# Kernel optimization log

Hardware: AMD Instinct MI355X
Metric: run time of the kernel (lower is better)

The kernel has to match this reference:

```python
import jax, jax.numpy as jnp
import numpy as np

B, N, D = 8, 256, 42   # batch, natoms, nFeatures
H1, H2 = 64, 32        # dmirror_FC hidden sizes


def setup_inputs() -> dict:
    key = jax.random.key(0)
    ks = jax.random.split(key, 8)
    s1, s2, s3 = (1.0 / np.sqrt(D)), (1.0 / np.sqrt(H1)), (1.0 / np.sqrt(H2))
    return {
        "image": jax.random.normal(ks[0], (B, N, D), dtype=jnp.float32),
        "dfeat": jax.random.normal(ks[1], (B, N, N, D, 3), dtype=jnp.float32),
        "W1": jax.random.normal(ks[2], (D, H1), dtype=jnp.float32) * s1,
        "b1": jax.random.normal(ks[3], (H1,), dtype=jnp.float32) * s1,
        "W2": jax.random.normal(ks[4], (H1, H2), dtype=jnp.float32) * s2,
        "b2": jax.random.normal(ks[5], (H2,), dtype=jnp.float32) * s2,
        "W3": jax.random.normal(ks[6], (H2, 1), dtype=jnp.float32) * s3,
        "b3": jax.random.normal(ks[7], (1,), dtype=jnp.float32) * s3,
    }


def reference(image, dfeat, W1, b1, W2, b2, W3, b3):
    # Per-atom mirrored MLP (dmirror_FC, softplus activation, d(softplus)=sigmoid),
    # fully vectorized over (batch, atom) instead of nested Python loops.
    z1 = image @ W1 + b1                 # [B,N,H1]
    a1 = jax.nn.softplus(z1)
    z2 = a1 @ W2 + b2                    # [B,N,H2]
    a2 = jax.nn.softplus(z2)
    Ei = (a2 @ W3 + b3)[..., 0]          # [B,N]
    Etot = jnp.sum(Ei, axis=1)           # [B]

    # Analytic mirrored backward: dEi/dFeat via chain rule
    g2 = jax.nn.sigmoid(z2) * W3[:, 0]   # [B,N,H2]
    g1 = jax.nn.sigmoid(z1) * (g2 @ W2.T)  # [B,N,H1]
    dEi_dFeat = g1 @ W1.T                # [B,N,D]

    # Force[b,i,:] = dEtot_dFeat[b] @ dfeat[b,i].reshape(N*D,3)
    Force = jnp.einsum('bjf,bijfc->bic', dEi_dFeat, dfeat)  # [B,N,3]
    return Etot, Force
```

## Files before the change

### kernel.cpp

```cpp
#include <hip/hip_runtime.h>

#define BATCH 8
#define NATOM 256
#define DF    42
#define H1    64
#define H2    32

__device__ __forceinline__ float softplus_f(float z) {
  return fmaxf(z, 0.f) + log1pf(expf(-fabsf(z)));
}

__global__ __launch_bounds__(256) void k1_mlp(
    const float* __restrict__ image,
    const float* __restrict__ W1, const float* __restrict__ b1,
    const float* __restrict__ W2, const float* __restrict__ b2,
    const float* __restrict__ W3, const float* __restrict__ b3,
    float* __restrict__ dG, float* __restrict__ Ei_ws) {
  __shared__ float sW1 [DF*H1];
  __shared__ float sW1T[H1*DF];
  __shared__ float sW2 [H1*H2];
  __shared__ float sW2T[H2*H1];
  __shared__ float sW3[H2], sb1[H1], sb2[H2];

  const int tid = threadIdx.x;
  for (int idx = tid; idx < DF*H1; idx += 256) {
    float w = W1[idx];
    sW1[idx] = w;
    sW1T[(idx & (H1-1))*DF + (idx >> 6)] = w;
  }
  for (int idx = tid; idx < H1*H2; idx += 256) {
    float w = W2[idx];
    sW2[idx] = w;
    sW2T[(idx & (H2-1))*H1 + (idx >> 5)] = w;
  }
  if (tid < H2)                    { sW3[tid] = W3[tid]; sb2[tid] = b2[tid]; }
  else if (tid >= 64 && tid < 128) { sb1[tid-64] = b1[tid-64]; }
  __syncthreads();

  const int lane = tid & 63;
  const int atom = blockIdx.x * 4 + (tid >> 6);

  float xv = (lane < DF) ? image[atom*DF + lane] : 0.f;

  float z1 = sb1[lane];
  #pragma unroll
  for (int d = 0; d < DF; ++d)
    z1 = fmaf(__shfl(xv, d), sW1[d*H1 + lane], z1);
  float a1 = softplus_f(z1);

  const int h2l = lane & (H2-1);
  float z2 = sb2[h2l];
  #pragma unroll
  for (int h = 0; h < H1; ++h)
    z2 = fmaf(__shfl(a1, h), sW2[h*H2 + h2l], z2);
  float a2 = softplus_f(z2);

  float w3  = sW3[h2l];
  float eip = a2 * w3;
  #pragma unroll
  for (int off = 16; off; off >>= 1) eip += __shfl_xor(eip, off);
  float g2 = (1.f - expf(-a2)) * w3;

  float t1 = 0.f;
  #pragma unroll
  for (int h2 = 0; h2 < H2; ++h2)
    t1 = fmaf(__shfl(g2, h2), sW2T[h2*H1 + lane], t1);
  float g1 = (1.f - expf(-a1)) * t1;

  const int dl = (lane < DF) ? lane : 0;
  float s = 0.f;
  #pragma unroll
  for (int h = 0; h < H1; ++h)
    s = fmaf(__shfl(g1, h), sW1T[h*DF + dl], s);

  if (lane < DF) dG[atom*DF + lane] = s;
  if (lane == 0) Ei_ws[atom] = eip + b3[0];
}

__global__ __launch_bounds__(256) void k2_force(
    const float* __restrict__ dfeat,
    const float* __restrict__ dG,
    const float* __restrict__ Ei_ws,
    float* __restrict__ out) {
  __shared__ float4 dg4[NATOM*DF/4];
  __shared__ float red[4][3];
  __shared__ float ered[4];

  const int tid = threadIdx.x;
  const int bid = blockIdx.x;
  const int b = bid >> 8;
  const int i = bid & 255;

  const float4* __restrict__ dgg = (const float4*)(dG + b*(NATOM*DF));
  for (int idx = tid; idx < NATOM*DF/4; idx += 256)
    dg4[idx] = dgg[idx];

  if (i == 0) {
    float e = Ei_ws[b*NATOM + tid];
    #pragma unroll
    for (int off = 32; off; off >>= 1) e += __shfl_down(e, off);
    if ((tid & 63) == 0) ered[tid >> 6] = e;
  }
  __syncthreads();
  if (i == 0 && tid == 0) out[b] = ered[0] + ered[1] + ered[2] + ered[3];

  const float4* __restrict__ p4 =
      (const float4*)(dfeat + (size_t)bid * (NATOM*DF*3));

  float ax = 0.f, ay = 0.f, az = 0.f;
  for (int u = tid; u < NATOM*DF*3/12; u += 256) {
    float4 v0 = p4[3*u + 0];
    float4 v1 = p4[3*u + 1];
    float4 v2 = p4[3*u + 2];
    float4 g  = dg4[u];
    ax += g.x*v0.x + g.y*v0.w + g.z*v1.z + g.w*v2.y;
    ay += g.x*v0.y + g.y*v1.x + g.z*v1.w + g.w*v2.z;
    az += g.x*v0.z + g.y*v1.y + g.z*v2.x + g.w*v2.w;
  }

  #pragma unroll
  for (int off = 32; off; off >>= 1) {
    ax += __shfl_down(ax, off);
    ay += __shfl_down(ay, off);
    az += __shfl_down(az, off);
  }
  const int wv = tid >> 6;
  if ((tid & 63) == 0) { red[wv][0] = ax; red[wv][1] = ay; red[wv][2] = az; }
  __syncthreads();
  if (tid == 0) {
    out[BATCH + (size_t)bid*3 + 0] = red[0][0]+red[1][0]+red[2][0]+red[3][0];
    out[BATCH + (size_t)bid*3 + 1] = red[0][1]+red[1][1]+red[2][1]+red[3][1];
    out[BATCH + (size_t)bid*3 + 2] = red[0][2]+red[1][2]+red[2][2]+red[3][2];
  }
}

extern "C" void kernel_launch(void* const* d_in, const int* in_sizes, int n_in,
                              void* d_out, int out_size, void* d_ws, size_t ws_size,
                              hipStream_t stream) {
  const float* image = (const float*)d_in[0];
  const float* dfeat = (const float*)d_in[1];
  const float* W1    = (const float*)d_in[2];
  const float* b1    = (const float*)d_in[3];
  const float* W2    = (const float*)d_in[4];
  const float* b2    = (const float*)d_in[5];
  const float* W3    = (const float*)d_in[6];
  const float* b3    = (const float*)d_in[7];
  float* out = (float*)d_out;

  float* dG = (float*)d_ws;
  float* Ei = dG + BATCH*NATOM*DF;

  k1_mlp<<<BATCH*NATOM/4, 256, 0, stream>>>(image, W1, b1, W2, b2, W3, b3, dG, Ei);
  k2_force<<<BATCH*NATOM, 256, 0, stream>>>(dfeat, dG, Ei, out);
}
```

Baseline: 62.72 us.

## Drop LDS staging of dG in force kernel, use nontemporal dfeat loads

Removes the per-block copy of the batch's dG vector into shared memory (43 KB) and the barrier that followed it; each thread now reads its dG slice directly from global/L2. The dfeat stream is read with nontemporal loads so it does not evict dG from cache, and the loop is fixed-count with a tail and unrolled by two. Dropping the large LDS allocation and adding launch bounds of 8 aims to raise occupancy for this bandwidth-bound streaming kernel. In exchange, every block re-reads dG from L2 instead of LDS, and the Etot write moves after the final barrier.

```diff
diff --git a/kernel.cpp b/kernel.cpp
--- a/kernel.cpp
+++ b/kernel.cpp
@@ -5,6 +5,8 @@
 #define DF    42
 #define H1    64
 #define H2    32
+
+typedef float f32x4 __attribute__((ext_vector_type(4)));
 
 __device__ __forceinline__ float softplus_f(float z) {
   return fmaxf(z, 0.f) + log1pf(expf(-fabsf(z)));
@@ -77,12 +79,11 @@
   if (lane == 0) Ei_ws[atom] = eip + b3[0];
 }
 
-__global__ __launch_bounds__(256) void k2_force(
+__global__ __launch_bounds__(256, 8) void k2_force(
     const float* __restrict__ dfeat,
     const float* __restrict__ dG,
     const float* __restrict__ Ei_ws,
     float* __restrict__ out) {
-  __shared__ float4 dg4[NATOM*DF/4];
   __shared__ float red[4][3];
   __shared__ float ered[4];
 
@@ -91,28 +92,35 @@
   const int b = bid >> 8;
   const int i = bid & 255;
 
-  const float4* __restrict__ dgg = (const float4*)(dG + b*(NATOM*DF));
-  for (int idx = tid; idx < NATOM*DF/4; idx += 256)
-    dg4[idx] = dgg[idx];
-
   if (i == 0) {
     float e = Ei_ws[b*NATOM + tid];
     #pragma unroll
     for (int off = 32; off; off >>= 1) e += __shfl_down(e, off);
     if ((tid & 63) == 0) ered[tid >> 6] = e;
   }
-  __syncthreads();
-  if (i == 0 && tid == 0) out[b] = ered[0] + ered[1] + ered[2] + ered[3];
 
-  const float4* __restrict__ p4 =
-      (const float4*)(dfeat + (size_t)bid * (NATOM*DF*3));
+  const f32x4* __restrict__ dgg = (const f32x4*)(dG + b*(NATOM*DF));
+  const f32x4* __restrict__ p4 =
+      (const f32x4*)(dfeat + (size_t)bid * (NATOM*DF*3));
 
   float ax = 0.f, ay = 0.f, az = 0.f;
-  for (int u = tid; u < NATOM*DF*3/12; u += 256) {
-    float4 v0 = p4[3*u + 0];
-    float4 v1 = p4[3*u + 1];
-    float4 v2 = p4[3*u + 2];
-    float4 g  = dg4[u];
+  #pragma unroll 2
+  for (int it = 0; it < 10; ++it) {
+    const int u = tid + it * 256;
+    f32x4 v0 = __builtin_nontemporal_load(p4 + 3*u + 0);
+    f32x4 v1 = __builtin_nontemporal_load(p4 + 3*u + 1);
+    f32x4 v2 = __builtin_nontemporal_load(p4 + 3*u + 2);
+    f32x4 g  = dgg[u];
+    ax += g.x*v0.x + g.y*v0.w + g.z*v1.z + g.w*v2.y;
+    ay += g.x*v0.y + g.y*v1.x + g.z*v1.w + g.w*v2.z;
+    az += g.x*v0.z + g.y*v1.y + g.z*v2.x + g.w*v2.w;
+  }
+  if (tid < 128) {
+    const int u = tid + 2560;
+    f32x4 v0 = __builtin_nontemporal_load(p4 + 3*u + 0);
+    f32x4 v1 = __builtin_nontemporal_load(p4 + 3*u + 1);
+    f32x4 v2 = __builtin_nontemporal_load(p4 + 3*u + 2);
+    f32x4 g  = dgg[u];
     ax += g.x*v0.x + g.y*v0.w + g.z*v1.z + g.w*v2.y;
     ay += g.x*v0.y + g.y*v1.x + g.z*v1.w + g.w*v2.z;
     az += g.x*v0.z + g.y*v1.y + g.z*v2.x + g.w*v2.w;
@@ -131,6 +139,7 @@
     out[BATCH + (size_t)bid*3 + 0] = red[0][0]+red[1][0]+red[2][0]+red[3][0];
     out[BATCH + (size_t)bid*3 + 1] = red[0][1]+red[1][1]+red[2][1]+red[3][1];
     out[BATCH + (size_t)bid*3 + 2] = red[0][2]+red[1][2]+red[2][2]+red[3][2];
+    if (i == 0) out[b] = ered[0] + ered[1] + ered[2] + ered[3];
   }
 }
 
```

New measurement: 78.66 us. +25.4%, slower.

## Process four force rows per 512-thread block to amortize dG shared staging

Applied to the files above, without the earlier changes.

The force kernel now uses 512-thread blocks, and each block computes four atoms' force rows instead of one. The per-batch dG vector is staged into LDS once per four rows, which cuts the repeated LDS staging and dG reads. Inner loops are fully unrolled with fixed trip counts, and a per-row wave reduction writes into a larger shared buffer. The grid shrinks to a quarter of the blocks, which may reduce latency hiding on a memory-bound streaming load of dfeat.

```diff
diff --git a/kernel.cpp b/kernel.cpp
--- a/kernel.cpp
+++ b/kernel.cpp
@@ -5,6 +5,8 @@
 #define DF    42
 #define H1    64
 #define H2    32
+
+typedef float f32x4 __attribute__((ext_vector_type(4)));
 
 __device__ __forceinline__ float softplus_f(float z) {
   return fmaxf(z, 0.f) + log1pf(expf(-fabsf(z)));
@@ -77,61 +79,80 @@
   if (lane == 0) Ei_ws[atom] = eip + b3[0];
 }
 
-__global__ __launch_bounds__(256) void k2_force(
+__global__ __launch_bounds__(512, 4) void k2_force(
     const float* __restrict__ dfeat,
     const float* __restrict__ dG,
     const float* __restrict__ Ei_ws,
     float* __restrict__ out) {
-  __shared__ float4 dg4[NATOM*DF/4];
-  __shared__ float red[4][3];
+  __shared__ f32x4 dgL[NATOM*DF/4];
+  __shared__ float red[4][8][3];
   __shared__ float ered[4];
 
   const int tid = threadIdx.x;
-  const int bid = blockIdx.x;
-  const int b = bid >> 8;
-  const int i = bid & 255;
+  const int blk = blockIdx.x;
+  const int b = blk >> 6;
 
-  const float4* __restrict__ dgg = (const float4*)(dG + b*(NATOM*DF));
-  for (int idx = tid; idx < NATOM*DF/4; idx += 256)
-    dg4[idx] = dgg[idx];
+  const f32x4* __restrict__ dgg = (const f32x4*)(dG + b*(NATOM*DF));
+  #pragma unroll
+  for (int m = 0; m < 5; ++m) dgL[tid + m*512] = dgg[tid + m*512];
+  if (tid < 128) dgL[tid + 2560] = dgg[tid + 2560];
 
-  if (i == 0) {
+  if ((blk & 63) == 0 && tid < 256) {
     float e = Ei_ws[b*NATOM + tid];
     #pragma unroll
     for (int off = 32; off; off >>= 1) e += __shfl_down(e, off);
     if ((tid & 63) == 0) ered[tid >> 6] = e;
   }
   __syncthreads();
-  if (i == 0 && tid == 0) out[b] = ered[0] + ered[1] + ered[2] + ered[3];
 
-  const float4* __restrict__ p4 =
-      (const float4*)(dfeat + (size_t)bid * (NATOM*DF*3));
+  const int wv = tid >> 6;
+  for (int r = 0; r < 4; ++r) {
+    const int R = blk*4 + r;
+    const f32x4* __restrict__ p4 = (const f32x4*)(dfeat + (size_t)R * (NATOM*DF*3));
 
-  float ax = 0.f, ay = 0.f, az = 0.f;
-  for (int u = tid; u < NATOM*DF*3/12; u += 256) {
-    float4 v0 = p4[3*u + 0];
-    float4 v1 = p4[3*u + 1];
-    float4 v2 = p4[3*u + 2];
-    float4 g  = dg4[u];
-    ax += g.x*v0.x + g.y*v0.w + g.z*v1.z + g.w*v2.y;
-    ay += g.x*v0.y + g.y*v1.x + g.z*v1.w + g.w*v2.z;
-    az += g.x*v0.z + g.y*v1.y + g.z*v2.x + g.w*v2.w;
+    float ax = 0.f, ay = 0.f, az = 0.f;
+    #pragma unroll
+    for (int m = 0; m < 5; ++m) {
+      const int g = tid + m*512;
+      f32x4 v0 = p4[3*g + 0];
+      f32x4 v1 = p4[3*g + 1];
+      f32x4 v2 = p4[3*g + 2];
+      f32x4 gg = dgL[g];
+      ax += gg.x*v0.x + gg.y*v0.w + gg.z*v1.z + gg.w*v2.y;
+      ay += gg.x*v0.y + gg.y*v1.x + gg.z*v1.w + gg.w*v2.z;
+      az += gg.x*v0.z + gg.y*v1.y + gg.z*v2.x + gg.w*v2.w;
+    }
+    if (tid < 128) {
+      const int g = tid + 2560;
+      f32x4 v0 = p4[3*g + 0];
+      f32x4 v1 = p4[3*g + 1];
+      f32x4 v2 = p4[3*g + 2];
+      f32x4 gg = dgL[g];
+      ax += gg.x*v0.x + gg.y*v0.w + gg.z*v1.z + gg.w*v2.y;
+      ay += gg.x*v0.y + gg.y*v1.x + gg.z*v1.w + gg.w*v2.z;
+      az += gg.x*v0.z + gg.y*v1.y + gg.z*v2.x + gg.w*v2.w;
+    }
+
+    #pragma unroll
+    for (int off = 32; off; off >>= 1) {
+      ax += __shfl_down(ax, off);
+      ay += __shfl_down(ay, off);
+      az += __shfl_down(az, off);
+    }
+    if ((tid & 63) == 0) { red[r][wv][0] = ax; red[r][wv][1] = ay; red[r][wv][2] = az; }
   }
 
-  #pragma unroll
-  for (int off = 32; off; off >>= 1) {
-    ax += __shfl_down(ax, off);
-    ay += __shfl_down(ay, off);
-    az += __shfl_down(az, off);
+  __syncthreads();
+  if (tid < 12) {
+    const int r = tid >> 2 == 0 ? tid / 3 : tid / 3;
+    const int c = tid - (tid/3)*3;
+    float s = 0.f;
+    #pragma unroll
+    for (int w = 0; w < 8; ++w) s += red[tid/3][w][c];
+    out[BATCH + (size_t)(blk*4 + tid/3)*3 + c] = s;
   }
-  const int wv = tid >> 6;
-  if ((tid & 63) == 0) { red[wv][0] = ax; red[wv][1] = ay; red[wv][2] = az; }
-  __syncthreads();
-  if (tid == 0) {
-    out[BATCH + (size_t)bid*3 + 0] = red[0][0]+red[1][0]+red[2][0]+red[3][0];
-    out[BATCH + (size_t)bid*3 + 1] = red[0][1]+red[1][1]+red[2][1]+red[3][1];
-    out[BATCH + (size_t)bid*3 + 2] = red[0][2]+red[1][2]+red[2][2]+red[3][2];
-  }
+  if ((blk & 63) == 0 && tid == 12)
+    out[b] = ered[0] + ered[1] + ered[2] + ered[3];
 }
 
 extern "C" void kernel_launch(void* const* d_in, const int* in_sizes, int n_in,
@@ -151,5 +172,5 @@
   float* Ei = dG + BATCH*NATOM*DF;
 
   k1_mlp<<<BATCH*NATOM/4, 256, 0, stream>>>(image, W1, b1, W2, b2, W3, b3, dG, Ei);
-  k2_force<<<BATCH*NATOM, 256, 0, stream>>>(dfeat, dG, Ei, out);
+  k2_force<<<BATCH*NATOM/4, 512, 0, stream>>>(dfeat, dG, Ei, out);
 }
```

New measurement: 57.37 us. -8.5%, faster.
